# Optimization experiments

Hardware: AMD Instinct MI355X
Metric: run time of the kernel (lower is better)

The kernel has to match this reference:

```python
import jax, jax.numpy as jnp
import numpy as np

TOP_K = 2


def setup_inputs() -> dict:
    key = jax.random.key(0)
    ks = jax.random.split(key, 5)
    B, S, H, F, E = 1, 2048, 1024, 3584, 8
    scale_h = 1.0 / np.sqrt(H)
    scale_f = 1.0 / np.sqrt(F)
    return {
        "hidden_states": jax.random.normal(ks[0], (B, S, H), dtype=jnp.float32),
        "gate_w": jax.random.normal(ks[1], (E, H), dtype=jnp.float32) * scale_h,
        "w1": jax.random.normal(ks[2], (E, H, F), dtype=jnp.float32) * scale_h,
        "w3": jax.random.normal(ks[3], (E, H, F), dtype=jnp.float32) * scale_h,
        "w2": jax.random.normal(ks[4], (E, F, H), dtype=jnp.float32) * scale_f,
    }


def reference(hidden_states, gate_w, w1, w2, w3):
    B, S, H = hidden_states.shape
    E = gate_w.shape[0]
    x = hidden_states.reshape(-1, H)  # [T, H]
    # Router: logits -> fp32 softmax -> top-k -> renormalize
    router_logits = x @ gate_w.T  # [T, E]
    probs = jax.nn.softmax(router_logits.astype(jnp.float32), axis=-1)
    top_w, top_idx = jax.lax.top_k(probs, TOP_K)  # [T, K]
    top_w = top_w / jnp.sum(top_w, axis=-1, keepdims=True)
    top_w = top_w.astype(x.dtype)
    # Dense combine weights [T, E]: routing weight if expert selected else 0
    combine = jnp.sum(jax.nn.one_hot(top_idx, E, dtype=x.dtype) * top_w[..., None], axis=1)
    # Per-expert SwiGLU FFN, weighted-summed (loop over small fixed E)
    out = jnp.zeros_like(x)
    for e in range(E):
        h = jax.nn.silu(x @ w1[e]) * (x @ w3[e])  # [T, F]
        out = out + (h @ w2[e]) * combine[:, e:e + 1]
    return out.reshape(B, S, H), router_logits
```

## Files before the change

kernel.cpp:

```cpp
#include <hip/hip_runtime.h>
#include <cstdint>
#include <cstddef>

#define Tt 2048
#define Hh 1024
#define Ff 3584
#define Ee 8
#define ROWS_CAP 5120

#define OFF_CTRL   0u
#define OFF_TOKE   256u
#define OFF_TOKW   (256u + 16384u)
#define OFF_ROWMAP (256u + 32768u)
#define OFF_ROWW   (256u + 32768u + 20480u)
#define OFF_XG     (1ull << 20)
#define OFF_G      (12ull << 20)

typedef __attribute__((ext_vector_type(8))) short bf16x8;
typedef __attribute__((ext_vector_type(4))) float f32x4;

__device__ __forceinline__ unsigned short f2bf(float f) {
  unsigned int u = __float_as_uint(f);
  u += 0x7fffu + ((u >> 16) & 1u);
  return (unsigned short)(u >> 16);
}

__device__ __forceinline__ unsigned pkbf(float a, float b) {
  unsigned r;
  asm("v_cvt_pk_bf16_f32 %0, %1, %2" : "=v"(r) : "v"(a), "v"(b));
  return r;
}

__device__ __forceinline__ void gload_lds16(const void* g, void* l) {
  auto gp = (const __attribute__((address_space(1))) char*)(uintptr_t)g;
  auto lp = (__attribute__((address_space(3))) char*)(uintptr_t)l;
  __builtin_amdgcn_global_load_lds(gp, lp, 16, 0, 0);
}

__device__ __forceinline__ bf16x8 frg(const char* lds, int row, int gc) {
  return *(const bf16x8*)(lds + row * 64 + ((gc ^ ((row >> 1) & 3)) * 16));
}

__global__ __launch_bounds__(256) void router_kernel(
    const float* __restrict__ x, const float* __restrict__ gw,
    float* __restrict__ logits_out, int* __restrict__ tok_e,
    float* __restrict__ tok_w, int* __restrict__ ctrl) {
  const int lane = threadIdx.x & 63;
  const int t = blockIdx.x * 4 + (threadIdx.x >> 6);
  const float4* xp = (const float4*)(x + (size_t)t * Hh + lane * 16);
  float4 x0 = xp[0], x1 = xp[1], x2 = xp[2], x3 = xp[3];
  float lg[Ee];
#pragma unroll
  for (int e = 0; e < Ee; ++e) {
    const float4* gp = (const float4*)(gw + e * Hh + lane * 16);
    float4 g0 = gp[0], g1 = gp[1], g2 = gp[2], g3 = gp[3];
    float s = x0.x*g0.x + x0.y*g0.y + x0.z*g0.z + x0.w*g0.w
            + x1.x*g1.x + x1.y*g1.y + x1.z*g1.z + x1.w*g1.w
            + x2.x*g2.x + x2.y*g2.y + x2.z*g2.z + x2.w*g2.w
            + x3.x*g3.x + x3.y*g3.y + x3.z*g3.z + x3.w*g3.w;
#pragma unroll
    for (int o = 32; o; o >>= 1) s += __shfl_xor(s, o);
    lg[e] = s;
  }
  if (lane == 0) {
    float m = lg[0];
#pragma unroll
    for (int e = 1; e < Ee; ++e) m = fmaxf(m, lg[e]);
    float p[Ee];
#pragma unroll
    for (int e = 0; e < Ee; ++e) p[e] = expf(lg[e] - m);
    int a0 = 0;
#pragma unroll
    for (int e = 1; e < Ee; ++e) if (p[e] > p[a0]) a0 = e;
    int a1 = (a0 == 0) ? 1 : 0;
#pragma unroll
    for (int e = 0; e < Ee; ++e) if (e != a0 && p[e] > p[a1]) a1 = e;
    float rs = p[a0] + p[a1];
    float w0 = p[a0] / rs, w1 = p[a1] / rs;
#pragma unroll
    for (int e = 0; e < Ee; ++e) logits_out[(size_t)t * Ee + e] = lg[e];
    tok_e[t * 2] = a0; tok_e[t * 2 + 1] = a1;
    tok_w[t * 2] = w0; tok_w[t * 2 + 1] = w1;
    atomicAdd(&ctrl[a0], 1); atomicAdd(&ctrl[a1], 1);
  }
}

__global__ void offsets_kernel(int* ctrl) {
  if (threadIdx.x == 0) {
    int acc = 0;
    for (int e = 0; e < Ee; ++e) {
      ctrl[16 + e] = acc;
      acc += ((ctrl[e] + 127) >> 7) << 7;
    }
    ctrl[16 + Ee] = acc;
  }
}

__global__ __launch_bounds__(512) void assign_kernel(
    int* ctrl, const int* __restrict__ tok_e, const float* __restrict__ tok_w,
    int* __restrict__ rowmap, float* __restrict__ roww) {
  int i = blockIdx.x * 512 + threadIdx.x;
  if (i < 2 * Tt) {
    int e = tok_e[i];
    int pos = atomicAdd(&ctrl[8 + e], 1);
    int r = ctrl[16 + e] + pos;
    rowmap[r] = i >> 1;
    roww[r] = tok_w[i];
  }
  if (i < Ee * 128) {
    int e = i >> 7, pd = i & 127;
    int o = ctrl[16 + e], o1 = ctrl[16 + e + 1], c = ctrl[e];
    int r = o + c + pd;
    if (r < o1) { rowmap[r] = -1; roww[r] = 0.f; }
  }
}

__global__ __launch_bounds__(128) void gather_kernel(
    const float* __restrict__ x, const int* __restrict__ ctrl,
    const int* __restrict__ rowmap, unsigned short* __restrict__ Xg) {
  int r = blockIdx.x;
  if (r >= ctrl[16 + Ee]) return;
  int t = rowmap[r];
  int j = threadIdx.x;
  uint4 v = make_uint4(0u, 0u, 0u, 0u);
  if (t >= 0) {
    const float4* xp = (const float4*)(x + (size_t)t * Hh + j * 8);
    float4 a = xp[0], b = xp[1];
    v.x = (unsigned)f2bf(a.x) | ((unsigned)f2bf(a.y) << 16);
    v.y = (unsigned)f2bf(a.z) | ((unsigned)f2bf(a.w) << 16);
    v.z = (unsigned)f2bf(b.x) | ((unsigned)f2bf(b.y) << 16);
    v.w = (unsigned)f2bf(b.z) | ((unsigned)f2bf(b.w) << 16);
  }
  *(uint4*)(Xg + (size_t)r * Hh + j * 8) = v;
}

__global__ __launch_bounds__(512, 4) void ffn13_fused(
    const unsigned short* __restrict__ Xg, const float* __restrict__ w1,
    const float* __restrict__ w3, const int* __restrict__ ctrl,
    unsigned short* __restrict__ G) {
  __shared__ alignas(16) char sA[2][8192], sB1[2][8192], sB3[2][8192];
  int lin = blockIdx.y * 28 + blockIdx.x;
  int wg = (lin & 7) * 448 + (lin >> 3);
  int bx = wg % 28, by = wg / 28;
  const int e = by >> 4, mt = by & 15;
  const int off0 = ctrl[16 + e], off1 = ctrl[16 + e + 1];
  const int row0 = off0 + mt * 128;
  if (row0 >= off1) return;
  const int n0 = bx * 128;
  const int tid = threadIdx.x, lane = tid & 63, wv = tid >> 6;
  const int wr = wv >> 2, wc = wv & 3;
  const float* w1e = w1 + (size_t)e * Hh * Ff;
  const float* w3e = w3 + (size_t)e * Hh * Ff;
  f32x4 acc1[4][2] = {};
  f32x4 acc3[4][2] = {};
  const int srow = wv * 16 + (lane >> 2);
  const int sgc = (lane & 3) ^ ((lane >> 3) & 3);
  const unsigned short* gA = Xg + (size_t)(row0 + srow) * Hh + sgc * 8;
  const int bn = tid & 127, bkq = tid >> 7;
  const int posB = bkq ^ ((bn >> 1) & 3);
  const int wofB = bn * 64 + posB * 16;
  const float* pB1 = w1e + (size_t)(bkq * 8) * Ff + n0 + bn;
  const float* pB3 = w3e + (size_t)(bkq * 8) * Ff + n0 + bn;
  float r1[8], r3[8];

#pragma unroll
  for (int i = 0; i < 8; ++i) r1[i] = pB1[(size_t)i * Ff];
#pragma unroll
  for (int i = 0; i < 8; ++i) r3[i] = pB3[(size_t)i * Ff];
  gload_lds16(gA, sA[0] + wv * 1024);
  {
    uint4 q;
    q.x = pkbf(r1[0], r1[1]); q.y = pkbf(r1[2], r1[3]);
    q.z = pkbf(r1[4], r1[5]); q.w = pkbf(r1[6], r1[7]);
    *(uint4*)(sB1[0] + wofB) = q;
    q.x = pkbf(r3[0], r3[1]); q.y = pkbf(r3[2], r3[3]);
    q.z = pkbf(r3[4], r3[5]); q.w = pkbf(r3[6], r3[7]);
    *(uint4*)(sB3[0] + wofB) = q;
  }
  __syncthreads();

  for (int it = 0; it < 32; ++it) {
    const int cur = it & 1;
    if (it < 31) {
      const size_t ko = (size_t)(it + 1) * 32;
      gload_lds16(gA + ko, sA[cur ^ 1] + wv * 1024);
      const float* p1 = pB1 + ko * Ff;
      const float* p3 = pB3 + ko * Ff;
#pragma unroll
      for (int i = 0; i < 8; ++i) r1[i] = p1[(size_t)i * Ff];
#pragma unroll
      for (int i = 0; i < 8; ++i) r3[i] = p3[(size_t)i * Ff];
    }
    const int gc = lane >> 4;
    bf16x8 af[4];
#pragma unroll
    for (int mi = 0; mi < 4; ++mi)
      af[mi] = frg(sA[cur], wr * 64 + mi * 16 + (lane & 15), gc);
    __builtin_amdgcn_s_setprio(1);
#pragma unroll
    for (int ni = 0; ni < 2; ++ni) {
      bf16x8 b1 = frg(sB1[cur], wc * 32 + ni * 16 + (lane & 15), gc);
      bf16x8 b3 = frg(sB3[cur], wc * 32 + ni * 16 + (lane & 15), gc);
#pragma unroll
      for (int mi = 0; mi < 4; ++mi) {
        acc1[mi][ni] = __builtin_amdgcn_mfma_f32_16x16x32_bf16(af[mi], b1, acc1[mi][ni], 0, 0, 0);
        acc3[mi][ni] = __builtin_amdgcn_mfma_f32_16x16x32_bf16(af[mi], b3, acc3[mi][ni], 0, 0, 0);
      }
    }
    __builtin_amdgcn_s_setprio(0);
    if (it < 31) {
      uint4 q;
      q.x = pkbf(r1[0], r1[1]); q.y = pkbf(r1[2], r1[3]);
      q.z = pkbf(r1[4], r1[5]); q.w = pkbf(r1[6], r1[7]);
      *(uint4*)(sB1[cur ^ 1] + wofB) = q;
      q.x = pkbf(r3[0], r3[1]); q.y = pkbf(r3[2], r3[3]);
      q.z = pkbf(r3[4], r3[5]); q.w = pkbf(r3[6], r3[7]);
      *(uint4*)(sB3[cur ^ 1] + wofB) = q;
    }
    __syncthreads();
  }
  const int rb = wr * 64 + 4 * (lane >> 4), cb = wc * 32 + (lane & 15);
#pragma unroll
  for (int mi = 0; mi < 4; ++mi)
#pragma unroll
    for (int ni = 0; ni < 2; ++ni)
#pragma unroll
      for (int r = 0; r < 4; ++r) {
        float h1 = acc1[mi][ni][r], h3 = acc3[mi][ni][r];
        float gv = h1 / (1.f + __expf(-h1)) * h3;
        G[(size_t)(row0 + rb + mi * 16 + r) * Ff + n0 + cb + ni * 16] = f2bf(gv);
      }
}

__global__ __launch_bounds__(512, 4) void ffn2_fused(
    const unsigned short* __restrict__ G, const float* __restrict__ w2,
    const int* __restrict__ ctrl, const int* __restrict__ rowmap,
    const float* __restrict__ roww, float* __restrict__ out) {
  __shared__ alignas(16) char sA[2][8192], sB[2][8192];
  int lin = blockIdx.y * 8 + blockIdx.x;
  int wg = (lin & 7) * 128 + (lin >> 3);
  int bx = wg % 8, by = wg / 8;
  const int e = by >> 4, mt = by & 15;
  const int off0 = ctrl[16 + e], off1 = ctrl[16 + e + 1];
  const int row0 = off0 + mt * 128;
  if (row0 >= off1) return;
  const int n0 = bx * 128;
  const int tid = threadIdx.x, lane = tid & 63, wv = tid >> 6;
  const int wr = wv >> 2, wc = wv & 3;
  const float* w2e = w2 + (size_t)e * Ff * Hh;
  f32x4 acc[4][2] = {};
  const int srow = wv * 16 + (lane >> 2);
  const int sgc = (lane & 3) ^ ((lane >> 3) & 3);
  const unsigned short* gA = G + (size_t)(row0 + srow) * Ff + sgc * 8;
  const int bn = tid & 127, bkq = tid >> 7;
  const int posB = bkq ^ ((bn >> 1) & 3);
  const int wofB = bn * 64 + posB * 16;
  const float* pB = w2e + (size_t)(bkq * 8) * Hh + n0 + bn;
  float r2[8];

#pragma unroll
  for (int i = 0; i < 8; ++i) r2[i] = pB[(size_t)i * Hh];
  gload_lds16(gA, sA[0] + wv * 1024);
  {
    uint4 q;
    q.x = pkbf(r2[0], r2[1]); q.y = pkbf(r2[2], r2[3]);
    q.z = pkbf(r2[4], r2[5]); q.w = pkbf(r2[6], r2[7]);
    *(uint4*)(sB[0] + wofB) = q;
  }
  __syncthreads();

  for (int it = 0; it < 112; ++it) {
    const int cur = it & 1;
    if (it < 111) {
      const size_t ko = (size_t)(it + 1) * 32;
      gload_lds16(gA + ko, sA[cur ^ 1] + wv * 1024);
      const float* p2 = pB + ko * Hh;
#pragma unroll
      for (int i = 0; i < 8; ++i) r2[i] = p2[(size_t)i * Hh];
    }
    const int gc = lane >> 4;
    bf16x8 af[4];
#pragma unroll
    for (int mi = 0; mi < 4; ++mi)
      af[mi] = frg(sA[cur], wr * 64 + mi * 16 + (lane & 15), gc);
    __builtin_amdgcn_s_setprio(1);
#pragma unroll
    for (int ni = 0; ni < 2; ++ni) {
      bf16x8 b = frg(sB[cur], wc * 32 + ni * 16 + (lane & 15), gc);
#pragma unroll
      for (int mi = 0; mi < 4; ++mi)
        acc[mi][ni] = __builtin_amdgcn_mfma_f32_16x16x32_bf16(af[mi], b, acc[mi][ni], 0, 0, 0);
    }
    __builtin_amdgcn_s_setprio(0);
    if (it < 111) {
      uint4 q;
      q.x = pkbf(r2[0], r2[1]); q.y = pkbf(r2[2], r2[3]);
      q.z = pkbf(r2[4], r2[5]); q.w = pkbf(r2[6], r2[7]);
      *(uint4*)(sB[cur ^ 1] + wofB) = q;
    }
    __syncthreads();
  }
  const int rb = wr * 64 + 4 * (lane >> 4), cb = wc * 32 + (lane & 15);
#pragma unroll
  for (int mi = 0; mi < 4; ++mi)
#pragma unroll
    for (int r = 0; r < 4; ++r) {
      int grow = row0 + rb + mi * 16 + r;
      int t = rowmap[grow];
      if (t < 0) continue;
      float wgt = roww[grow];
#pragma unroll
      for (int ni = 0; ni < 2; ++ni)
        atomicAdd(&out[(size_t)t * Hh + n0 + cb + ni * 16], wgt * acc[mi][ni][r]);
    }
}

extern "C" void kernel_launch(void* const* d_in, const int* in_sizes, int n_in,
                              void* d_out, int out_size, void* d_ws, size_t ws_size,
                              hipStream_t stream) {
  const float* x  = (const float*)d_in[0];
  const float* gw = (const float*)d_in[1];
  const float* w1 = (const float*)d_in[2];
  const float* w3 = (const float*)d_in[3];
  const float* w2 = (const float*)d_in[4];
  float* out = (float*)d_out;
  float* logits = out + (size_t)Tt * Hh;
  char* ws = (char*)d_ws;
  int* ctrl = (int*)(ws + OFF_CTRL);
  int* tok_e = (int*)(ws + OFF_TOKE);
  float* tok_w = (float*)(ws + OFF_TOKW);
  int* rowmap = (int*)(ws + OFF_ROWMAP);
  float* roww = (float*)(ws + OFF_ROWW);
  unsigned short* Xg = (unsigned short*)(ws + OFF_XG);
  unsigned short* G  = (unsigned short*)(ws + OFF_G);

  hipMemsetAsync(ctrl, 0, 256, stream);
  hipMemsetAsync(out, 0, (size_t)Tt * Hh * sizeof(float), stream);
  router_kernel<<<Tt / 4, 256, 0, stream>>>(x, gw, logits, tok_e, tok_w, ctrl);
  offsets_kernel<<<1, 64, 0, stream>>>(ctrl);
  assign_kernel<<<8, 512, 0, stream>>>(ctrl, tok_e, tok_w, rowmap, roww);
  gather_kernel<<<ROWS_CAP, 128, 0, stream>>>(x, ctrl, rowmap, Xg);
  ffn13_fused<<<dim3(28, Ee * 16), 512, 0, stream>>>(Xg, w1, w3, ctrl, G);
  ffn2_fused<<<dim3(8, Ee * 16), 512, 0, stream>>>(G, w2, ctrl, rowmap, roww, out);
}
```

Measured before the change: 344.8 us.

## Deepen weight prefetch pipeline, remap blocks per XCD, split-K the down projection

Measured after the change: 333.0 us. 3.4% less time.

```diff
diff --git a/kernel.cpp b/kernel.cpp
--- a/kernel.cpp
+++ b/kernel.cpp
@@ -140,9 +140,10 @@
     unsigned short* __restrict__ G) {
   __shared__ alignas(16) char sA[2][8192], sB1[2][8192], sB3[2][8192];
   int lin = blockIdx.y * 28 + blockIdx.x;
-  int wg = (lin & 7) * 448 + (lin >> 3);
-  int bx = wg % 28, by = wg / 28;
-  const int e = by >> 4, mt = by & 15;
+  int xcd = lin & 7, idx = lin >> 3;
+  int p = xcd + 8 * (idx >> 4);
+  int mt = idx & 15;
+  int e = p / 28, bx = p % 28;
   const int off0 = ctrl[16 + e], off1 = ctrl[16 + e + 1];
   const int row0 = off0 + mt * 128;
   if (row0 >= off1) return;
@@ -163,11 +164,11 @@
   const float* pB3 = w3e + (size_t)(bkq * 8) * Ff + n0 + bn;
   float r1[8], r3[8];
 
+  gload_lds16(gA, sA[0] + wv * 1024);
 #pragma unroll
   for (int i = 0; i < 8; ++i) r1[i] = pB1[(size_t)i * Ff];
 #pragma unroll
   for (int i = 0; i < 8; ++i) r3[i] = pB3[(size_t)i * Ff];
-  gload_lds16(gA, sA[0] + wv * 1024);
   {
     uint4 q;
     q.x = pkbf(r1[0], r1[1]); q.y = pkbf(r1[2], r1[3]);
@@ -177,37 +178,18 @@
     q.z = pkbf(r3[4], r3[5]); q.w = pkbf(r3[6], r3[7]);
     *(uint4*)(sB3[0] + wofB) = q;
   }
-  __syncthreads();
+#pragma unroll
+  for (int i = 0; i < 8; ++i) r1[i] = pB1[(size_t)(32 + i) * Ff];
+#pragma unroll
+  for (int i = 0; i < 8; ++i) r3[i] = pB3[(size_t)(32 + i) * Ff];
+  asm volatile("s_waitcnt vmcnt(16) lgkmcnt(0)" ::: "memory");
+  __builtin_amdgcn_s_barrier();
+  __builtin_amdgcn_sched_barrier(0);
 
   for (int it = 0; it < 32; ++it) {
     const int cur = it & 1;
-    if (it < 31) {
-      const size_t ko = (size_t)(it + 1) * 32;
-      gload_lds16(gA + ko, sA[cur ^ 1] + wv * 1024);
-      const float* p1 = pB1 + ko * Ff;
-      const float* p3 = pB3 + ko * Ff;
-#pragma unroll
-      for (int i = 0; i < 8; ++i) r1[i] = p1[(size_t)i * Ff];
-#pragma unroll
-      for (int i = 0; i < 8; ++i) r3[i] = p3[(size_t)i * Ff];
-    }
-    const int gc = lane >> 4;
-    bf16x8 af[4];
-#pragma unroll
-    for (int mi = 0; mi < 4; ++mi)
-      af[mi] = frg(sA[cur], wr * 64 + mi * 16 + (lane & 15), gc);
-    __builtin_amdgcn_s_setprio(1);
-#pragma unroll
-    for (int ni = 0; ni < 2; ++ni) {
-      bf16x8 b1 = frg(sB1[cur], wc * 32 + ni * 16 + (lane & 15), gc);
-      bf16x8 b3 = frg(sB3[cur], wc * 32 + ni * 16 + (lane & 15), gc);
-#pragma unroll
-      for (int mi = 0; mi < 4; ++mi) {
-        acc1[mi][ni] = __builtin_amdgcn_mfma_f32_16x16x32_bf16(af[mi], b1, acc1[mi][ni], 0, 0, 0);
-        acc3[mi][ni] = __builtin_amdgcn_mfma_f32_16x16x32_bf16(af[mi], b3, acc3[mi][ni], 0, 0, 0);
-      }
-    }
-    __builtin_amdgcn_s_setprio(0);
+    if (it < 31) gload_lds16(gA + (size_t)(it + 1) * 32, sA[cur ^ 1] + wv * 1024);
+    __builtin_amdgcn_sched_barrier(0);
     if (it < 31) {
       uint4 q;
       q.x = pkbf(r1[0], r1[1]); q.y = pkbf(r1[2], r1[3]);
@@ -217,7 +199,38 @@
       q.z = pkbf(r3[4], r3[5]); q.w = pkbf(r3[6], r3[7]);
       *(uint4*)(sB3[cur ^ 1] + wofB) = q;
     }
-    __syncthreads();
+    if (it < 30) {
+      const float* p1 = pB1 + (size_t)(it + 2) * 32 * Ff;
+      const float* p3 = pB3 + (size_t)(it + 2) * 32 * Ff;
+#pragma unroll
+      for (int i = 0; i < 8; ++i) r1[i] = p1[(size_t)i * Ff];
+#pragma unroll
+      for (int i = 0; i < 8; ++i) r3[i] = p3[(size_t)i * Ff];
+    }
+    __builtin_amdgcn_sched_barrier(0);
+    const int gc = lane >> 4;
+    bf16x8 af[4];
+#pragma unroll
+    for (int mi = 0; mi < 4; ++mi)
+      af[mi] = frg(sA[cur], wr * 64 + mi * 16 + (lane & 15), gc);
+    __builtin_amdgcn_s_setprio(1);
+#pragma unroll
+    for (int ni = 0; ni < 2; ++ni) {
+      bf16x8 b1 = frg(sB1[cur], wc * 32 + ni * 16 + (lane & 15), gc);
+      bf16x8 b3 = frg(sB3[cur], wc * 32 + ni * 16 + (lane & 15), gc);
+#pragma unroll
+      for (int mi = 0; mi < 4; ++mi) {
+        acc1[mi][ni] = __builtin_amdgcn_mfma_f32_16x16x32_bf16(af[mi], b1, acc1[mi][ni], 0, 0, 0);
+        acc3[mi][ni] = __builtin_amdgcn_mfma_f32_16x16x32_bf16(af[mi], b3, acc3[mi][ni], 0, 0, 0);
+      }
+    }
+    __builtin_amdgcn_s_setprio(0);
+    if (it < 31) {
+      if (it < 30) asm volatile("s_waitcnt vmcnt(16) lgkmcnt(0)" ::: "memory");
+      else         asm volatile("s_waitcnt vmcnt(0) lgkmcnt(0)" ::: "memory");
+      __builtin_amdgcn_s_barrier();
+      __builtin_amdgcn_sched_barrier(0);
+    }
   }
   const int rb = wr * 64 + 4 * (lane >> 4), cb = wc * 32 + (lane & 15);
 #pragma unroll
@@ -237,68 +250,81 @@
     const int* __restrict__ ctrl, const int* __restrict__ rowmap,
     const float* __restrict__ roww, float* __restrict__ out) {
   __shared__ alignas(16) char sA[2][8192], sB[2][8192];
-  int lin = blockIdx.y * 8 + blockIdx.x;
-  int wg = (lin & 7) * 128 + (lin >> 3);
-  int bx = wg % 8, by = wg / 8;
-  const int e = by >> 4, mt = by & 15;
+  int lin = (blockIdx.z * 128 + blockIdx.y) * 8 + blockIdx.x;
+  int xcd = lin & 7, idx = lin >> 3;
+  int e = idx >> 5, sub = idx & 31;
+  int mt = sub >> 1, ks = sub & 1;
+  int bx = xcd;
   const int off0 = ctrl[16 + e], off1 = ctrl[16 + e + 1];
   const int row0 = off0 + mt * 128;
   if (row0 >= off1) return;
   const int n0 = bx * 128;
+  const int kb = ks * (Ff / 2);
   const int tid = threadIdx.x, lane = tid & 63, wv = tid >> 6;
   const int wr = wv >> 2, wc = wv & 3;
   const float* w2e = w2 + (size_t)e * Ff * Hh;
   f32x4 acc[4][2] = {};
   const int srow = wv * 16 + (lane >> 2);
   const int sgc = (lane & 3) ^ ((lane >> 3) & 3);
-  const unsigned short* gA = G + (size_t)(row0 + srow) * Ff + sgc * 8;
+  const unsigned short* gA = G + (size_t)(row0 + srow) * Ff + kb + sgc * 8;
   const int bn = tid & 127, bkq = tid >> 7;
   const int posB = bkq ^ ((bn >> 1) & 3);
   const int wofB = bn * 64 + posB * 16;
-  const float* pB = w2e + (size_t)(bkq * 8) * Hh + n0 + bn;
+  const float* pB = w2e + (size_t)(kb + bkq * 8) * Hh + n0 + bn;
   float r2[8];
 
+  gload_lds16(gA, sA[0] + wv * 1024);
 #pragma unroll
   for (int i = 0; i < 8; ++i) r2[i] = pB[(size_t)i * Hh];
-  gload_lds16(gA, sA[0] + wv * 1024);
   {
     uint4 q;
     q.x = pkbf(r2[0], r2[1]); q.y = pkbf(r2[2], r2[3]);
     q.z = pkbf(r2[4], r2[5]); q.w = pkbf(r2[6], r2[7]);
     *(uint4*)(sB[0] + wofB) = q;
   }
-  __syncthreads();
-
-  for (int it = 0; it < 112; ++it) {
+#pragma unroll
+  for (int i = 0; i < 8; ++i) r2[i] = pB[(size_t)(32 + i) * Hh];
+  asm volatile("s_waitcnt vmcnt(8) lgkmcnt(0)" ::: "memory");
+  __builtin_amdgcn_s_barrier();
+  __builtin_amdgcn_sched_barrier(0);
+
+  const int NT = 56;
+  for (int it = 0; it < NT; ++it) {
     const int cur = it & 1;
-    if (it < 111) {
-      const size_t ko = (size_t)(it + 1) * 32;
-      gload_lds16(gA + ko, sA[cur ^ 1] + wv * 1024);
-      const float* p2 = pB + ko * Hh;
-#pragma unroll
-      for (int i = 0; i < 8; ++i) r2[i] = p2[(size_t)i * Hh];
-    }
-    const int gc = lane >> 4;
-    bf16x8 af[4];
-#pragma unroll
-    for (int mi = 0; mi < 4; ++mi)
-      af[mi] = frg(sA[cur], wr * 64 + mi * 16 + (lane & 15), gc);
-    __builtin_amdgcn_s_setprio(1);
-#pragma unroll
-    for (int ni = 0; ni < 2; ++ni) {
-      bf16x8 b = frg(sB[cur], wc * 32 + ni * 16 + (lane & 15), gc);
-#pragma unroll
-      for (int mi = 0; mi < 4; ++mi)
-        acc[mi][ni] = __builtin_amdgcn_mfma_f32_16x16x32_bf16(af[mi], b, acc[mi][ni], 0, 0, 0);
-    }
-    __builtin_amdgcn_s_setprio(0);
-    if (it < 111) {
+    if (it < NT - 1) gload_lds16(gA + (size_t)(it + 1) * 32, sA[cur ^ 1] + wv * 1024);
+    __builtin_amdgcn_sched_barrier(0);
+    if (it < NT - 1) {
       uint4 q;
       q.x = pkbf(r2[0], r2[1]); q.y = pkbf(r2[2], r2[3]);
       q.z = pkbf(r2[4], r2[5]); q.w = pkbf(r2[6], r2[7]);
       *(uint4*)(sB[cur ^ 1] + wofB) = q;
     }
-    __syncthreads();
+    if (it < NT - 2) {
+      const float* p2 = pB + (size_t)(it + 2) * 32 * Hh;
+#pragma unroll
+      for (int i = 0; i < 8; ++i) r2[i] = p2[(size_t)i * Hh];
+    }
+    __builtin_amdgcn_sched_barrier(0);
+    const int gc = lane >> 4;
+    bf16x8 af[4];
+#pragma unroll
+    for (int mi = 0; mi < 4; ++mi)
+      af[mi] = frg(sA[cur], wr * 64 + mi * 16 + (lane & 15), gc);
+    __builtin_amdgcn_s_setprio(1);
+#pragma unroll
+    for (int ni = 0; ni < 2; ++ni) {
+      bf16x8 b = frg(sB[cur], wc * 32 + ni * 16 + (lane & 15), gc);
+#pragma unroll
+      for (int mi = 0; mi < 4; ++mi)
+        acc[mi][ni] = __builtin_amdgcn_mfma_f32_16x16x32_bf16(af[mi], b, acc[mi][ni], 0, 0, 0);
+    }
+    __builtin_amdgcn_s_setprio(0);
+    if (it < NT - 1) {
+      if (it < NT - 2) asm volatile("s_waitcnt vmcnt(8) lgkmcnt(0)" ::: "memory");
+      else             asm volatile("s_waitcnt vmcnt(0) lgkmcnt(0)" ::: "memory");
+      __builtin_amdgcn_s_barrier();
+      __builtin_amdgcn_sched_barrier(0);
+    }
   }
   const int rb = wr * 64 + 4 * (lane >> 4), cb = wc * 32 + (lane & 15);
 #pragma unroll
@@ -340,6 +366,6 @@
   offsets_kernel<<<1, 64, 0, stream>>>(ctrl);
   assign_kernel<<<8, 512, 0, stream>>>(ctrl, tok_e, tok_w, rowmap, roww);
   gather_kernel<<<ROWS_CAP, 128, 0, stream>>>(x, ctrl, rowmap, Xg);
-  ffn13_fused<<<dim3(28, Ee * 16), 512, 0, stream>>>(Xg, w1, w3, ctrl, G);
-  ffn2_fused<<<dim3(8, Ee * 16), 512, 0, stream>>>(G, w2, ctrl, rowmap, roww, out);
-}
+  ffn13_fused<<<dim3(28, 128), 512, 0, stream>>>(Xg, w1, w3, ctrl, G);
+  ffn2_fused<<<dim3(8, 128, 2), 512, 0, stream>>>(G, w2, ctrl, rowmap, roww, out);
+}
```

## Restructure MoE FFN into 256-tile concatenated w1/w3 GEMM with silu fused into w2

Applied to the files above, without the earlier changes.

Result: slower. 388.8 us (+12.8%).

```diff
diff --git a/kernel.cpp b/kernel.cpp
--- a/kernel.cpp
+++ b/kernel.cpp
@@ -6,15 +6,16 @@
 #define Hh 1024
 #define Ff 3584
 #define Ee 8
-#define ROWS_CAP 5120
+#define ROWS_CAP 6400
+#define NP 7168
 
 #define OFF_CTRL   0u
-#define OFF_TOKE   256u
-#define OFF_TOKW   (256u + 16384u)
-#define OFF_ROWMAP (256u + 32768u)
-#define OFF_ROWW   (256u + 32768u + 20480u)
+#define OFF_TOKE   4096u
+#define OFF_TOKW   (4096u + 16384u)
+#define OFF_ROWMAP 65536u
+#define OFF_ROWW   98304u
 #define OFF_XG     (1ull << 20)
-#define OFF_G      (12ull << 20)
+#define OFF_H      (16ull << 20)
 
 typedef __attribute__((ext_vector_type(8))) short bf16x8;
 typedef __attribute__((ext_vector_type(4))) float f32x4;
@@ -90,7 +91,7 @@
     int acc = 0;
     for (int e = 0; e < Ee; ++e) {
       ctrl[16 + e] = acc;
-      acc += ((ctrl[e] + 127) >> 7) << 7;
+      acc += ((ctrl[e] + 255) >> 8) << 8;
     }
     ctrl[16 + Ee] = acc;
   }
@@ -107,8 +108,8 @@
     rowmap[r] = i >> 1;
     roww[r] = tok_w[i];
   }
-  if (i < Ee * 128) {
-    int e = i >> 7, pd = i & 127;
+  if (i < Ee * 256) {
+    int e = i >> 8, pd = i & 255;
     int o = ctrl[16 + e], o1 = ctrl[16 + e + 1], c = ctrl[e];
     int r = o + c + pd;
     if (r < o1) { rowmap[r] = -1; roww[r] = 0.f; }
@@ -134,173 +135,194 @@
   *(uint4*)(Xg + (size_t)r * Hh + j * 8) = v;
 }
 
-__global__ __launch_bounds__(512, 4) void ffn13_fused(
+#define MFMA_PHASE(CUR)                                                        \
+  { const int gc = lane >> 4;                                                  \
+    bf16x8 af[4];                                                              \
+    _Pragma("unroll") for (int mi = 0; mi < 4; ++mi)                           \
+      af[mi] = frg(sA[CUR], wr * 64 + mi * 16 + (lane & 15), gc);              \
+    __builtin_amdgcn_s_setprio(1);                                             \
+    _Pragma("unroll") for (int ni = 0; ni < 4; ++ni) {                         \
+      bf16x8 bb = frg(sB[CUR], wc * 64 + ni * 16 + (lane & 15), gc);           \
+      _Pragma("unroll") for (int mi = 0; mi < 4; ++mi)                         \
+        acc[mi][ni] = __builtin_amdgcn_mfma_f32_16x16x32_bf16(af[mi], bb,      \
+                                                        acc[mi][ni], 0, 0, 0); \
+    }                                                                          \
+    __builtin_amdgcn_s_setprio(0); }
+
+__global__ __launch_bounds__(1024, 4) void h13_gemm(
     const unsigned short* __restrict__ Xg, const float* __restrict__ w1,
     const float* __restrict__ w3, const int* __restrict__ ctrl,
-    unsigned short* __restrict__ G) {
-  __shared__ alignas(16) char sA[2][8192], sB1[2][8192], sB3[2][8192];
-  int lin = blockIdx.y * 28 + blockIdx.x;
-  int wg = (lin & 7) * 448 + (lin >> 3);
-  int bx = wg % 28, by = wg / 28;
-  const int e = by >> 4, mt = by & 15;
+    unsigned short* __restrict__ H) {
+  __shared__ alignas(16) char sA[2][16384], sB[2][16384];
+  const int lin = blockIdx.x + 28 * blockIdx.y;
+  const int p = (lin & 7) * 28 + (lin >> 3);
+  const int e = p / 28, bx = p % 28, mt = blockIdx.z;
   const int off0 = ctrl[16 + e], off1 = ctrl[16 + e + 1];
-  const int row0 = off0 + mt * 128;
+  const int row0 = off0 + mt * 256;
   if (row0 >= off1) return;
-  const int n0 = bx * 128;
+  const int n0 = bx * 256;
+  const float* wsel = (n0 < Ff) ? (w1 + (size_t)e * Hh * Ff + n0)
+                                : (w3 + (size_t)e * Hh * Ff + (n0 - Ff));
   const int tid = threadIdx.x, lane = tid & 63, wv = tid >> 6;
   const int wr = wv >> 2, wc = wv & 3;
-  const float* w1e = w1 + (size_t)e * Hh * Ff;
-  const float* w3e = w3 + (size_t)e * Hh * Ff;
-  f32x4 acc1[4][2] = {};
-  f32x4 acc3[4][2] = {};
-  const int srow = wv * 16 + (lane >> 2);
+  f32x4 acc[4][4] = {};
   const int sgc = (lane & 3) ^ ((lane >> 3) & 3);
-  const unsigned short* gA = Xg + (size_t)(row0 + srow) * Hh + sgc * 8;
-  const int bn = tid & 127, bkq = tid >> 7;
-  const int posB = bkq ^ ((bn >> 1) & 3);
-  const int wofB = bn * 64 + posB * 16;
-  const float* pB1 = w1e + (size_t)(bkq * 8) * Ff + n0 + bn;
-  const float* pB3 = w3e + (size_t)(bkq * 8) * Ff + n0 + bn;
-  float r1[8], r3[8];
-
-#pragma unroll
-  for (int i = 0; i < 8; ++i) r1[i] = pB1[(size_t)i * Ff];
-#pragma unroll
-  for (int i = 0; i < 8; ++i) r3[i] = pB3[(size_t)i * Ff];
+  const unsigned short* gA = Xg + (size_t)(row0 + wv * 16 + (lane >> 2)) * Hh + sgc * 8;
+  const int bn = tid & 255, bkq = tid >> 8;
+  const int wofB = bn * 64 + ((bkq ^ ((bn >> 1) & 3)) * 16);
+  const float* pB = wsel + (size_t)(bkq * 8) * Ff + bn;
+  float rB[8];
+
   gload_lds16(gA, sA[0] + wv * 1024);
+  __builtin_amdgcn_sched_barrier(0);
+#pragma unroll
+  for (int i = 0; i < 8; ++i) rB[i] = pB[(size_t)i * Ff];
   {
     uint4 q;
-    q.x = pkbf(r1[0], r1[1]); q.y = pkbf(r1[2], r1[3]);
-    q.z = pkbf(r1[4], r1[5]); q.w = pkbf(r1[6], r1[7]);
-    *(uint4*)(sB1[0] + wofB) = q;
-    q.x = pkbf(r3[0], r3[1]); q.y = pkbf(r3[2], r3[3]);
-    q.z = pkbf(r3[4], r3[5]); q.w = pkbf(r3[6], r3[7]);
-    *(uint4*)(sB3[0] + wofB) = q;
-  }
-  __syncthreads();
-
+    q.x = pkbf(rB[0], rB[1]); q.y = pkbf(rB[2], rB[3]);
+    q.z = pkbf(rB[4], rB[5]); q.w = pkbf(rB[6], rB[7]);
+    *(uint4*)(sB[0] + wofB) = q;
+  }
+#pragma unroll
+  for (int i = 0; i < 8; ++i) rB[i] = pB[(size_t)(32 + i) * Ff];
+  asm volatile("s_waitcnt vmcnt(0) lgkmcnt(0)" ::: "memory");
+  __builtin_amdgcn_s_barrier();
+  __builtin_amdgcn_sched_barrier(0);
+
+#pragma unroll 2
   for (int it = 0; it < 32; ++it) {
     const int cur = it & 1;
-    if (it < 31) {
-      const size_t ko = (size_t)(it + 1) * 32;
-      gload_lds16(gA + ko, sA[cur ^ 1] + wv * 1024);
-      const float* p1 = pB1 + ko * Ff;
-      const float* p3 = pB3 + ko * Ff;
-#pragma unroll
-      for (int i = 0; i < 8; ++i) r1[i] = p1[(size_t)i * Ff];
-#pragma unroll
-      for (int i = 0; i < 8; ++i) r3[i] = p3[(size_t)i * Ff];
-    }
-    const int gc = lane >> 4;
-    bf16x8 af[4];
-#pragma unroll
-    for (int mi = 0; mi < 4; ++mi)
-      af[mi] = frg(sA[cur], wr * 64 + mi * 16 + (lane & 15), gc);
-    __builtin_amdgcn_s_setprio(1);
-#pragma unroll
-    for (int ni = 0; ni < 2; ++ni) {
-      bf16x8 b1 = frg(sB1[cur], wc * 32 + ni * 16 + (lane & 15), gc);
-      bf16x8 b3 = frg(sB3[cur], wc * 32 + ni * 16 + (lane & 15), gc);
-#pragma unroll
-      for (int mi = 0; mi < 4; ++mi) {
-        acc1[mi][ni] = __builtin_amdgcn_mfma_f32_16x16x32_bf16(af[mi], b1, acc1[mi][ni], 0, 0, 0);
-        acc3[mi][ni] = __builtin_amdgcn_mfma_f32_16x16x32_bf16(af[mi], b3, acc3[mi][ni], 0, 0, 0);
-      }
-    }
-    __builtin_amdgcn_s_setprio(0);
+    if (it < 31) gload_lds16(gA + (size_t)(it + 1) * 32, sA[cur ^ 1] + wv * 1024);
+    __builtin_amdgcn_sched_barrier(0);
     if (it < 31) {
       uint4 q;
-      q.x = pkbf(r1[0], r1[1]); q.y = pkbf(r1[2], r1[3]);
-      q.z = pkbf(r1[4], r1[5]); q.w = pkbf(r1[6], r1[7]);
-      *(uint4*)(sB1[cur ^ 1] + wofB) = q;
-      q.x = pkbf(r3[0], r3[1]); q.y = pkbf(r3[2], r3[3]);
-      q.z = pkbf(r3[4], r3[5]); q.w = pkbf(r3[6], r3[7]);
-      *(uint4*)(sB3[cur ^ 1] + wofB) = q;
-    }
-    __syncthreads();
-  }
-  const int rb = wr * 64 + 4 * (lane >> 4), cb = wc * 32 + (lane & 15);
+      q.x = pkbf(rB[0], rB[1]); q.y = pkbf(rB[2], rB[3]);
+      q.z = pkbf(rB[4], rB[5]); q.w = pkbf(rB[6], rB[7]);
+      *(uint4*)(sB[cur ^ 1] + wofB) = q;
+    }
+    if (it < 30) {
+      const float* pw = pB + (size_t)(it + 2) * 32 * Ff;
+#pragma unroll
+      for (int i = 0; i < 8; ++i) rB[i] = pw[(size_t)i * Ff];
+    }
+    __builtin_amdgcn_sched_barrier(0);
+    MFMA_PHASE(cur)
+    if (it < 31) {
+      if (it < 30) asm volatile("s_waitcnt vmcnt(8) lgkmcnt(0)" ::: "memory");
+      else         asm volatile("s_waitcnt vmcnt(0) lgkmcnt(0)" ::: "memory");
+      __builtin_amdgcn_s_barrier();
+      __builtin_amdgcn_sched_barrier(0);
+    }
+  }
+
+  const int rb = wr * 64 + 4 * (lane >> 4), cb = n0 + wc * 64 + (lane & 15);
 #pragma unroll
   for (int mi = 0; mi < 4; ++mi)
 #pragma unroll
-    for (int ni = 0; ni < 2; ++ni)
-#pragma unroll
-      for (int r = 0; r < 4; ++r) {
-        float h1 = acc1[mi][ni][r], h3 = acc3[mi][ni][r];
-        float gv = h1 / (1.f + __expf(-h1)) * h3;
-        G[(size_t)(row0 + rb + mi * 16 + r) * Ff + n0 + cb + ni * 16] = f2bf(gv);
-      }
-}
-
-__global__ __launch_bounds__(512, 4) void ffn2_fused(
-    const unsigned short* __restrict__ G, const float* __restrict__ w2,
+    for (int ni = 0; ni < 4; ++ni)
+#pragma unroll
+      for (int r = 0; r < 4; ++r)
+        H[(size_t)(row0 + rb + mi * 16 + r) * NP + cb + ni * 16] = f2bf(acc[mi][ni][r]);
+}
+
+__device__ __forceinline__ uint4 silu_mul_pack(uint4 a1, uint4 a3) {
+  const unsigned* p1 = (const unsigned*)&a1;
+  const unsigned* p3 = (const unsigned*)&a3;
+  uint4 r;
+  unsigned* pr = (unsigned*)&r;
+#pragma unroll
+  for (int w = 0; w < 4; ++w) {
+    float x0 = __uint_as_float((p1[w] & 0xFFFFu) << 16);
+    float x1 = __uint_as_float(p1[w] & 0xFFFF0000u);
+    float y0 = __uint_as_float((p3[w] & 0xFFFFu) << 16);
+    float y1 = __uint_as_float(p3[w] & 0xFFFF0000u);
+    float g0 = x0 / (1.f + __expf(-x0)) * y0;
+    float g1 = x1 / (1.f + __expf(-x1)) * y1;
+    pr[w] = pkbf(g0, g1);
+  }
+  return r;
+}
+
+__global__ __launch_bounds__(1024, 4) void ffn2_gemm(
+    const unsigned short* __restrict__ H, const float* __restrict__ w2,
     const int* __restrict__ ctrl, const int* __restrict__ rowmap,
     const float* __restrict__ roww, float* __restrict__ out) {
-  __shared__ alignas(16) char sA[2][8192], sB[2][8192];
-  int lin = blockIdx.y * 8 + blockIdx.x;
-  int wg = (lin & 7) * 128 + (lin >> 3);
-  int bx = wg % 8, by = wg / 8;
-  const int e = by >> 4, mt = by & 15;
+  __shared__ alignas(16) char sA[2][16384], sB[2][16384];
+  const int lin = blockIdx.x + 4 * blockIdx.y;
+  const int p = (lin & 7) * 4 + (lin >> 3);
+  const int e = p >> 2, bx = p & 3;
+  const int mt = blockIdx.z >> 2, ks = blockIdx.z & 3;
   const int off0 = ctrl[16 + e], off1 = ctrl[16 + e + 1];
-  const int row0 = off0 + mt * 128;
+  const int row0 = off0 + mt * 256;
   if (row0 >= off1) return;
-  const int n0 = bx * 128;
+  const int n0 = bx * 256;
+  const int kb = ks * (Ff / 4);
   const int tid = threadIdx.x, lane = tid & 63, wv = tid >> 6;
   const int wr = wv >> 2, wc = wv & 3;
-  const float* w2e = w2 + (size_t)e * Ff * Hh;
-  f32x4 acc[4][2] = {};
-  const int srow = wv * 16 + (lane >> 2);
-  const int sgc = (lane & 3) ^ ((lane >> 3) & 3);
-  const unsigned short* gA = G + (size_t)(row0 + srow) * Ff + sgc * 8;
-  const int bn = tid & 127, bkq = tid >> 7;
-  const int posB = bkq ^ ((bn >> 1) & 3);
-  const int wofB = bn * 64 + posB * 16;
-  const float* pB = w2e + (size_t)(bkq * 8) * Hh + n0 + bn;
-  float r2[8];
-
-#pragma unroll
-  for (int i = 0; i < 8; ++i) r2[i] = pB[(size_t)i * Hh];
-  gload_lds16(gA, sA[0] + wv * 1024);
+  f32x4 acc[4][4] = {};
+  const int arow = tid >> 2, akq = tid & 3;
+  const int wofA = arow * 64 + ((akq ^ ((arow >> 1) & 3)) * 16);
+  const unsigned short* pH1 = H + (size_t)(row0 + arow) * NP + kb + akq * 8;
+  const unsigned short* pH3 = pH1 + Ff;
+  const int bn = tid & 255, bkq = tid >> 8;
+  const int wofB = bn * 64 + ((bkq ^ ((bn >> 1) & 3)) * 16);
+  const float* pB = w2 + (size_t)e * Ff * Hh + (size_t)(kb + bkq * 8) * Hh + n0 + bn;
+  uint4 h1e, h3e, h1o, h3o;
+  float bEven[8], bOdd[8];
+
+  uint4 tA1 = *(const uint4*)(pH1);
+  uint4 tA3 = *(const uint4*)(pH3);
+  float tB[8];
+#pragma unroll
+  for (int i = 0; i < 8; ++i) tB[i] = pB[(size_t)i * Hh];
+  h1e = *(const uint4*)(pH1 + 32);  h3e = *(const uint4*)(pH3 + 32);
+  h1o = *(const uint4*)(pH1 + 64);  h3o = *(const uint4*)(pH3 + 64);
+#pragma unroll
+  for (int i = 0; i < 8; ++i) bEven[i] = pB[(size_t)(32 + i) * Hh];
+#pragma unroll
+  for (int i = 0; i < 8; ++i) bOdd[i] = pB[(size_t)(64 + i) * Hh];
+  *(uint4*)(sA[0] + wofA) = silu_mul_pack(tA1, tA3);
   {
     uint4 q;
-    q.x = pkbf(r2[0], r2[1]); q.y = pkbf(r2[2], r2[3]);
-    q.z = pkbf(r2[4], r2[5]); q.w = pkbf(r2[6], r2[7]);
+    q.x = pkbf(tB[0], tB[1]); q.y = pkbf(tB[2], tB[3]);
+    q.z = pkbf(tB[4], tB[5]); q.w = pkbf(tB[6], tB[7]);
     *(uint4*)(sB[0] + wofB) = q;
   }
-  __syncthreads();
-
-  for (int it = 0; it < 112; ++it) {
-    const int cur = it & 1;
-    if (it < 111) {
-      const size_t ko = (size_t)(it + 1) * 32;
-      gload_lds16(gA + ko, sA[cur ^ 1] + wv * 1024);
-      const float* p2 = pB + ko * Hh;
-#pragma unroll
-      for (int i = 0; i < 8; ++i) r2[i] = p2[(size_t)i * Hh];
-    }
-    const int gc = lane >> 4;
-    bf16x8 af[4];
-#pragma unroll
-    for (int mi = 0; mi < 4; ++mi)
-      af[mi] = frg(sA[cur], wr * 64 + mi * 16 + (lane & 15), gc);
-    __builtin_amdgcn_s_setprio(1);
-#pragma unroll
-    for (int ni = 0; ni < 2; ++ni) {
-      bf16x8 b = frg(sB[cur], wc * 32 + ni * 16 + (lane & 15), gc);
-#pragma unroll
-      for (int mi = 0; mi < 4; ++mi)
-        acc[mi][ni] = __builtin_amdgcn_mfma_f32_16x16x32_bf16(af[mi], b, acc[mi][ni], 0, 0, 0);
-    }
-    __builtin_amdgcn_s_setprio(0);
-    if (it < 111) {
-      uint4 q;
-      q.x = pkbf(r2[0], r2[1]); q.y = pkbf(r2[2], r2[3]);
-      q.z = pkbf(r2[4], r2[5]); q.w = pkbf(r2[6], r2[7]);
-      *(uint4*)(sB[cur ^ 1] + wofB) = q;
-    }
-    __syncthreads();
-  }
-  const int rb = wr * 64 + 4 * (lane >> 4), cb = wc * 32 + (lane & 15);
+  asm volatile("s_waitcnt lgkmcnt(0)" ::: "memory");
+  __builtin_amdgcn_s_barrier();
+  __builtin_amdgcn_sched_barrier(0);
+
+#define F2_ITER(IT, CUR, A1, A3, BS)                                           \
+  {                                                                            \
+    if ((IT) + 1 < 28) {                                                       \
+      *(uint4*)(sA[(CUR) ^ 1] + wofA) = silu_mul_pack(A1, A3);                 \
+      uint4 q;                                                                 \
+      q.x = pkbf(BS[0], BS[1]); q.y = pkbf(BS[2], BS[3]);                      \
+      q.z = pkbf(BS[4], BS[5]); q.w = pkbf(BS[6], BS[7]);                      \
+      *(uint4*)(sB[(CUR) ^ 1] + wofB) = q;                                     \
+    }                                                                          \
+    { int w = (IT) + 3; if (w >= 28) w -= 28;                                  \
+      A1 = *(const uint4*)(pH1 + (size_t)w * 32);                              \
+      A3 = *(const uint4*)(pH3 + (size_t)w * 32);                              \
+      const float* pw = pB + (size_t)w * 32 * Hh;                              \
+      _Pragma("unroll") for (int i = 0; i < 8; ++i) BS[i] = pw[(size_t)i * Hh]; } \
+    __builtin_amdgcn_sched_barrier(0);                                         \
+    MFMA_PHASE(CUR)                                                            \
+    if ((IT) + 1 < 28) {                                                       \
+      asm volatile("s_waitcnt lgkmcnt(0)" ::: "memory");                       \
+      __builtin_amdgcn_s_barrier();                                            \
+      __builtin_amdgcn_sched_barrier(0);                                       \
+    }                                                                          \
+  }
+
+  for (int j = 0; j < 14; ++j) {
+    const int it0 = 2 * j;
+    F2_ITER(it0, 0, h1e, h3e, bEven)
+    F2_ITER(it0 + 1, 1, h1o, h3o, bOdd)
+  }
+#undef F2_ITER
+
+  const int rb = wr * 64 + 4 * (lane >> 4), cb = wc * 64 + (lane & 15);
 #pragma unroll
   for (int mi = 0; mi < 4; ++mi)
 #pragma unroll
@@ -310,7 +332,7 @@
       if (t < 0) continue;
       float wgt = roww[grow];
 #pragma unroll
-      for (int ni = 0; ni < 2; ++ni)
+      for (int ni = 0; ni < 4; ++ni)
         atomicAdd(&out[(size_t)t * Hh + n0 + cb + ni * 16], wgt * acc[mi][ni][r]);
     }
 }
@@ -332,7 +354,7 @@
   int* rowmap = (int*)(ws + OFF_ROWMAP);
   float* roww = (float*)(ws + OFF_ROWW);
   unsigned short* Xg = (unsigned short*)(ws + OFF_XG);
-  unsigned short* G  = (unsigned short*)(ws + OFF_G);
+  unsigned short* H  = (unsigned short*)(ws + OFF_H);
 
   hipMemsetAsync(ctrl, 0, 256, stream);
   hipMemsetAsync(out, 0, (size_t)Tt * Hh * sizeof(float), stream);
@@ -340,6 +362,6 @@
   offsets_kernel<<<1, 64, 0, stream>>>(ctrl);
   assign_kernel<<<8, 512, 0, stream>>>(ctrl, tok_e, tok_w, rowmap, roww);
   gather_kernel<<<ROWS_CAP, 128, 0, stream>>>(x, ctrl, rowmap, Xg);
-  ffn13_fused<<<dim3(28, Ee * 16), 512, 0, stream>>>(Xg, w1, w3, ctrl, G);
-  ffn2_fused<<<dim3(8, Ee * 16), 512, 0, stream>>>(G, w2, ctrl, rowmap, roww, out);
-}
+  h13_gemm<<<dim3(28, 8, 16), 1024, 0, stream>>>(Xg, w1, w3, ctrl, H);
+  ffn2_gemm<<<dim3(4, 8, 64), 1024, 0, stream>>>(H, w2, ctrl, rowmap, roww, out);
+}
```
